# Performance work log

Measured on AMD Instinct MI355X. Metric: run time of the kernel, lower is better.

Reference implementation:

```python
import jax, jax.numpy as jnp
import numpy as np

IN_DIM = 64
HIDDEN = 128
NUM_LAYERS = 2
N_NODES = 10000
N_EDGES = 160000
N_GRAPHS = 32


def _lin_params(key, fan_in, fan_out):
    kw, kb = jax.random.split(key)
    s = 1.0 / np.sqrt(fan_in)
    W = jax.random.uniform(kw, (fan_in, fan_out), jnp.float32, -s, s)
    b = jax.random.uniform(kb, (fan_out,), jnp.float32, -s, s)
    return W, b


def setup_inputs() -> dict:
    key = jax.random.key(0)
    ks = jax.random.split(key, 24)
    H = HIDDEN
    inp = {}
    inp["x1"] = jax.random.normal(ks[0], (N_NODES, IN_DIM), jnp.float32)
    inp["edge_index1"] = jax.random.randint(ks[1], (2, N_EDGES), 0, N_NODES)
    inp["batch1"] = jnp.sort(jax.random.randint(ks[2], (N_NODES,), 0, N_GRAPHS))
    inp["x2"] = jax.random.normal(ks[3], (N_NODES, IN_DIM), jnp.float32)
    inp["edge_index2"] = jax.random.randint(ks[4], (2, N_EDGES), 0, N_NODES)
    inp["batch2"] = jnp.sort(jax.random.randint(ks[5], (N_NODES,), 0, N_GRAPHS))
    # embedding: Linear(in_dim -> hidden)
    inp["W_emb"], inp["b_emb"] = _lin_params(ks[6], IN_DIM, H)
    # per-layer GEMBConv params, stacked over layers
    mW1, mb1, mW2, mb2, uW1, ub1, uW2, ub2 = [], [], [], [], [], [], [], []
    for l in range(NUM_LAYERS):
        k = jax.random.split(ks[7 + l], 4)
        W, b = _lin_params(k[0], 2 * H, 2 * H); mW1.append(W); mb1.append(b)
        W, b = _lin_params(k[1], 2 * H, 2 * H); mW2.append(W); mb2.append(b)
        W, b = _lin_params(k[2], 3 * H, 2 * H); uW1.append(W); ub1.append(b)
        W, b = _lin_params(k[3], 2 * H, H); uW2.append(W); ub2.append(b)
    inp["msg_W1"] = jnp.stack(mW1); inp["msg_b1"] = jnp.stack(mb1)
    inp["msg_W2"] = jnp.stack(mW2); inp["msg_b2"] = jnp.stack(mb2)
    inp["upd_W1"] = jnp.stack(uW1); inp["upd_b1"] = jnp.stack(ub1)
    inp["upd_W2"] = jnp.stack(uW2); inp["upd_b2"] = jnp.stack(ub2)
    # readout: node_net Linear(H -> 2H) (use_gate doubles), graph_net Linear(H -> H)
    inp["node_W"], inp["node_b"] = _lin_params(ks[20], H, 2 * H)
    inp["graph_W"], inp["graph_b"] = _lin_params(ks[21], H, H)
    return inp


def _genet_branch(x, edge_index, batch, W_emb, b_emb,
                  msg_W1, msg_b1, msg_W2, msg_b2,
                  upd_W1, upd_b1, upd_W2, upd_b2,
                  node_W, node_b, graph_W, graph_b):
    H = HIDDEN
    h = x @ W_emb + b_emb  # [N, H]
    tgt, src = edge_index[0], edge_index[1]
    for l in range(NUM_LAYERS):
        # gather-concat: (x[src], x[tgt]) -> [E, 2H]
        mi = jnp.concatenate([h[src], h[tgt]], axis=-1)
        m = jax.nn.relu(mi @ msg_W1[l] + msg_b1[l]) @ msg_W2[l] + msg_b2[l]
        agg = jax.ops.segment_sum(m, tgt, num_segments=N_NODES)  # [N, 2H]
        ui = jnp.concatenate([agg, h], axis=-1)  # [N, 3H]
        u = jax.nn.relu(ui @ upd_W1[l] + upd_b1[l]) @ upd_W2[l] + upd_b2[l]
        h = h + u  # residual node update
    nx = h @ node_W + node_b  # [N, 2H]
    gates = jax.nn.sigmoid(nx[:, :H])
    v = nx[:, H:] * gates
    g = jax.ops.segment_sum(v, batch, num_segments=N_GRAPHS)  # sum pool
    return g @ graph_W + graph_b  # [G, H]


def reference(x1, edge_index1, batch1, x2, edge_index2, batch2,
              W_emb, b_emb, msg_W1, msg_b1, msg_W2, msg_b2,
              upd_W1, upd_b1, upd_W2, upd_b2,
              node_W, node_b, graph_W, graph_b):
    args = (W_emb, b_emb, msg_W1, msg_b1, msg_W2, msg_b2,
            upd_W1, upd_b1, upd_W2, upd_b2, node_W, node_b, graph_W, graph_b)
    embed1 = _genet_branch(x1, edge_index1, batch1, *args)
    embed2 = _genet_branch(x2, edge_index2, batch2, *args)
    return (embed1, embed2)
```

## Files before the change

### kernel.cpp

```cpp
#include <hip/hip_runtime.h>

typedef unsigned short u16;
typedef __bf16 bf16x8 __attribute__((ext_vector_type(8)));
typedef float f32x4 __attribute__((ext_vector_type(4)));
typedef unsigned short u16x8 __attribute__((ext_vector_type(8)));

constexpr int NN  = 10000;
constexpr int NE  = 160000;
constexpr int NG  = 32;
constexpr int HD  = 128;

constexpr size_t WT_PQ   = 0;
constexpr size_t WT_M2R  = 262144;
constexpr size_t WT_UPD1 = 524288;
constexpr size_t WT_U1C  = 917504;
constexpr size_t WT_UPD2 = 1310720;
constexpr size_t WT_NODE = 1441792;
constexpr size_t OFF_C2  = 1507328;
constexpr size_t OFF_DEG = 1509376;
constexpr size_t OFF_ST  = 1589376;
constexpr size_t OFF_CUR = 1669440;
constexpr size_t OFF_SRC = 1749440;
constexpr size_t OFF_H   = 3029440;
constexpr size_t OFF_HB  = 13269440;
constexpr size_t OFF_PQ  = 18389440;
constexpr size_t OFF_UI  = 38869440;
constexpr size_t OFF_G   = 54229440;

__device__ inline u16 f2b(float f) {
  unsigned int u = __float_as_uint(f);
  unsigned int r = u + 0x7fffu + ((u >> 16) & 1u);
  return (u16)(r >> 16);
}
__device__ inline float b2f(u16 u) { return __uint_as_float(((unsigned int)u) << 16); }

__global__ __launch_bounds__(256) void k_prep(
    const float* msgW1, const float* msgW2, const float* updW1,
    const float* updW2, const float* nodeW, const float* msgb2,
    u16* tpq, u16* t2r, u16* t3, u16* tu1c, u16* t4, u16* t5,
    float* c2, int* deg, float* g) {
  int idx = blockIdx.x * 256 + threadIdx.x;
  if (idx < 131072) {
    int l = idx >> 16, r = idx & 65535, n = r >> 7, k = r & 127;
    int row = (n < 256) ? k : (128 + k);
    tpq[idx] = f2b(msgW1[l * 65536 + row * 256 + (n & 255)]);
    t2r[idx] = f2b(msgW2[idx]);
  }
  if (idx < 196608) {
    int l = idx / 98304, r = idx % 98304, n = r / 384, k = r % 384;
    t3[idx] = f2b(updW1[l * 98304 + k * 256 + n]);
  }
  if (idx < 65536) {
    int l = idx >> 15, r = idx & 32767, n = r >> 7, k = r & 127;
    tu1c[l * 98304 + n * 384 + 256 + k] = f2b(updW1[l * 98304 + (256 + k) * 256 + n]);
    int n2 = (idx & 32767) >> 8, k2 = idx & 255;
    t4[idx] = f2b(updW2[(idx >> 15) * 32768 + (k2 << 7) + n2]);
  }
  if (idx < 32768) {
    int n = idx >> 7, k = idx & 127;
    t5[idx] = f2b(nodeW[(k << 8) + n]);
  }
  if (idx < 512) {
    int l = idx >> 8, n = idx & 255;
    const float* b2 = msgb2 + l * 256;
    const float* U1 = updW1 + l * 98304 + n;
    float a = 0.f;
    for (int c = 0; c < 256; c++) a += b2[c] * U1[c * 256];
    c2[idx] = a;
  }
  if (idx < 2 * NN) deg[idx] = 0;
  if (idx < 2 * NG * 128) g[idx] = 0.f;
}

__global__ __launch_bounds__(256) void k_deg(const int* ei0, const int* ei1, int* deg) {
  int br = blockIdx.z;
  int e = blockIdx.x * 256 + threadIdx.x;
  if (e >= NE) return;
  const int* tgt = br ? ei1 : ei0;
  atomicAdd(deg + br * NN + tgt[e], 1);
}

__global__ __launch_bounds__(256) void k_scan(const int* deg, int* starts, int* cursor) {
  int br = blockIdx.z;
  const int* d = deg + br * NN;
  int* st = starts + br * (NN + 8);
  int* cu = cursor + br * NN;
  __shared__ int part[257];
  int t = threadIdx.x;
  int c0 = t * 40;
  int s = 0;
  for (int i = 0; i < 40; i++) if (c0 + i < NN) s += d[c0 + i];
  part[t] = s;
  __syncthreads();
  if (t == 0) {
    int run = 0;
    for (int i = 0; i < 256; i++) { int v = part[i]; part[i] = run; run += v; }
    part[256] = run;
  }
  __syncthreads();
  int run = part[t];
  for (int i = 0; i < 40; i++) {
    int n = c0 + i;
    if (n < NN) { st[n] = run; cu[n] = run; run += d[n]; }
  }
  if (t == 255) st[NN] = part[256];
}

__global__ __launch_bounds__(256) void k_scatter(const int* ei0, const int* ei1,
                                                 int* cursor, int* srcs) {
  int br = blockIdx.z;
  int e = blockIdx.x * 256 + threadIdx.x;
  if (e >= NE) return;
  const int* ei = br ? ei1 : ei0;
  int t = ei[e], s = ei[NE + e];
  int pos = atomicAdd(cursor + br * NN + t, 1);
  srcs[br * NE + pos] = s;
}

__global__ __launch_bounds__(256) void k_embed(
    const float* x1, const float* x2, const float* W, const float* b,
    float* h, u16* h_bf, u16* ui) {
  int br = blockIdx.z;
  const float* x = br ? x2 : x1;
  float* hB = h + (size_t)br * NN * HD;
  u16* hbB = h_bf + (size_t)br * NN * HD;
  u16* uiB = ui + (size_t)br * NN * 384;
  __shared__ float sW[64 * 128];
  __shared__ float sx[32 * 64];
  int tid = threadIdx.x;
  for (int i = tid; i < 64 * 128; i += 256) sW[i] = W[i];
  int r0 = blockIdx.x * 32;
  for (int i = tid; i < 32 * 64; i += 256) {
    int r = i >> 6, k = i & 63;
    sx[i] = (r0 + r < NN) ? x[(size_t)(r0 + r) * 64 + k] : 0.f;
  }
  __syncthreads();
  int c = tid & 127;
  int rbase = (tid >> 7) * 16;
  for (int r = rbase; r < rbase + 16; r++) {
    float acc = b[c];
#pragma unroll
    for (int k = 0; k < 64; k++) acc += sx[r * 64 + k] * sW[k * 128 + c];
    int gr = r0 + r;
    if (gr < NN) {
      u16 bv = f2b(acc);
      hB[(size_t)gr * HD + c] = acc;
      hbB[(size_t)gr * HD + c] = bv;
      uiB[(size_t)gr * 384 + 256 + c] = bv;
    }
  }
}

__global__ __launch_bounds__(256) void k_edge(const u16* PQ, const int* starts,
                                              const int* srcs, const float* b1, u16* ui) {
  int br = blockIdx.z;
  int node = blockIdx.x * 4 + (threadIdx.x >> 6);
  int lane = threadIdx.x & 63;
  int half = lane >> 5;
  int c0 = (lane & 31) * 8;
  const u16* PQb = PQ + (size_t)br * NN * 512;
  const int* st = starts + br * (NN + 8);
  const int* sr = srcs + br * NE;
  u16x8 qr = *(const u16x8*)(PQb + (size_t)node * 512 + 256 + c0);
  float qv[8], acc[8];
#pragma unroll
  for (int j = 0; j < 8; j++) { qv[j] = b2f(qr[j]) + b1[c0 + j]; acc[j] = 0.f; }
  int e0 = st[node], e1 = st[node + 1];
  int e = e0 + half;
  for (; e + 2 < e1; e += 4) {
    int s0 = sr[e], s1 = sr[e + 2];
    u16x8 p0 = *(const u16x8*)(PQb + (size_t)s0 * 512 + c0);
    u16x8 p1 = *(const u16x8*)(PQb + (size_t)s1 * 512 + c0);
#pragma unroll
    for (int j = 0; j < 8; j++) {
      float v0 = b2f(p0[j]) + qv[j];
      float v1 = b2f(p1[j]) + qv[j];
      acc[j] += (v0 > 0.f ? v0 : 0.f) + (v1 > 0.f ? v1 : 0.f);
    }
  }
  for (; e < e1; e += 2) {
    int s0 = sr[e];
    u16x8 p0 = *(const u16x8*)(PQb + (size_t)s0 * 512 + c0);
#pragma unroll
    for (int j = 0; j < 8; j++) {
      float v0 = b2f(p0[j]) + qv[j];
      acc[j] += (v0 > 0.f ? v0 : 0.f);
    }
  }
#pragma unroll
  for (int j = 0; j < 8; j++) acc[j] += __shfl_xor(acc[j], 32);
  if (half == 0) {
    u16x8 o;
#pragma unroll
    for (int j = 0; j < 8; j++) o[j] = f2b(acc[j]);
    *(u16x8*)(ui + (size_t)br * NN * 384 + (size_t)node * 384 + c0) = o;
  }
}

struct GemmP {
  const u16* A;   size_t sA;
  int lda;
  const u16* Wt;  size_t sW;
  u16* outb;  size_t s_outb;
  int M, N, K, ldo;
};

#define LSTR 40

__global__ __launch_bounds__(256) void k_gemm(GemmP p) {
  const int br = blockIdx.z;
  const int tid = threadIdx.x;
  const int lane = tid & 63, wave = tid >> 6;
  const int wm = (wave & 1) * 64, wn = (wave >> 1) * 64;
  const int q = lane >> 4, lr = lane & 15;
  const int m0 = blockIdx.x * 128, n0 = blockIdx.y * 128;
  __shared__ alignas(16) u16 lA[128 * LSTR];
  __shared__ alignas(16) u16 lB[128 * LSTR];

  f32x4 acc[4][4];
#pragma unroll
  for (int i = 0; i < 4; i++)
#pragma unroll
    for (int j = 0; j < 4; j++) acc[i][j] = (f32x4){0.f, 0.f, 0.f, 0.f};

  const u16* Abr = p.A + (size_t)br * p.sA;
  const u16* Wbr = p.Wt + (size_t)br * p.sW;

  for (int k0 = 0; k0 < p.K; k0 += 32) {
#pragma unroll
    for (int c = tid; c < 512; c += 256) {
      int r = c >> 2, kc = (c & 3) << 3;
      int gr = m0 + r;
      u16x8 v = {0, 0, 0, 0, 0, 0, 0, 0};
      if (gr < p.M) v = *(const u16x8*)(Abr + (size_t)gr * p.lda + k0 + kc);
      *(u16x8*)&lA[r * LSTR + kc] = v;
    }
#pragma unroll
    for (int c = tid; c < 512; c += 256) {
      int r = c >> 2, kc = (c & 3) << 3;
      *(u16x8*)&lB[r * LSTR + kc] = *(const u16x8*)(Wbr + (size_t)(n0 + r) * p.K + k0 + kc);
    }
    __syncthreads();
    bf16x8 af[4], bfr[4];
#pragma unroll
    for (int i = 0; i < 4; i++) af[i] = *(const bf16x8*)&lA[(wm + i * 16 + lr) * LSTR + q * 8];
#pragma unroll
    for (int i = 0; i < 4; i++) bfr[i] = *(const bf16x8*)&lB[(wn + i * 16 + lr) * LSTR + q * 8];
#pragma unroll
    for (int mi = 0; mi < 4; mi++)
#pragma unroll
      for (int ni = 0; ni < 4; ni++)
        acc[mi][ni] = __builtin_amdgcn_mfma_f32_16x16x32_bf16(af[mi], bfr[ni], acc[mi][ni], 0, 0, 0);
    __syncthreads();
  }

  u16* ob = p.outb + (size_t)br * p.s_outb;
#pragma unroll
  for (int mi = 0; mi < 4; mi++)
#pragma unroll
    for (int rg = 0; rg < 4; rg++) {
      int row = m0 + wm + mi * 16 + q * 4 + rg;
      if (row >= p.M) continue;
#pragma unroll
      for (int ni = 0; ni < 4; ni++) {
        int col = n0 + wn + ni * 16 + lr;
        ob[(size_t)row * p.ldo + col] = f2b(acc[mi][ni][rg]);
      }
    }
}

__global__ __launch_bounds__(256, 4) void k_upd(
    const u16* ui_all, const u16* w1c, const float* b1u, const float* c2l,
    const int* deg_all, const u16* w2, const float* b2u,
    float* h_all, u16* hb_all) {
  const int br = blockIdx.z;
  const int tid = threadIdx.x;
  const int lane = tid & 63, wave = tid >> 6;
  const int q = lane >> 4, lr = lane & 15;
  const int m0 = blockIdx.x * 32;

  __shared__ alignas(16) u16 sm[32 * LSTR + 256 * LSTR];
  u16* lA = sm;
  u16* lB = sm + 32 * LSTR;
  u16* lU = sm;

  const u16* ui = ui_all + (size_t)br * NN * 384;

  const int wn = wave * 64;
  f32x4 acc[2][4];
#pragma unroll
  for (int i = 0; i < 2; i++)
#pragma unroll
    for (int j = 0; j < 4; j++) acc[i][j] = (f32x4){0.f, 0.f, 0.f, 0.f};

  for (int k0 = 0; k0 < 384; k0 += 32) {
    for (int c = tid; c < 1152; c += 256) {
      if (c < 128) {
        int r = c >> 2, kc = (c & 3) << 3;
        int gr = m0 + r;
        u16x8 v = {0, 0, 0, 0, 0, 0, 0, 0};
        if (gr < NN) v = *(const u16x8*)(ui + (size_t)gr * 384 + k0 + kc);
        *(u16x8*)&lA[r * LSTR + kc] = v;
      } else {
        int cc = c - 128;
        int r = cc >> 2, kc = (cc & 3) << 3;
        *(u16x8*)&lB[r * LSTR + kc] = *(const u16x8*)(w1c + (size_t)r * 384 + k0 + kc);
      }
    }
    __syncthreads();
    bf16x8 af[2], bfr[4];
#pragma unroll
    for (int i = 0; i < 2; i++) af[i] = *(const bf16x8*)&lA[(i * 16 + lr) * LSTR + q * 8];
#pragma unroll
    for (int i = 0; i < 4; i++) bfr[i] = *(const bf16x8*)&lB[(wn + i * 16 + lr) * LSTR + q * 8];
#pragma unroll
    for (int mi = 0; mi < 2; mi++)
#pragma unroll
      for (int ni = 0; ni < 4; ni++)
        acc[mi][ni] = __builtin_amdgcn_mfma_f32_16x16x32_bf16(af[mi], bfr[ni], acc[mi][ni], 0, 0, 0);
    __syncthreads();
  }

  const int* deg = deg_all + br * NN;
#pragma unroll
  for (int mi = 0; mi < 2; mi++)
#pragma unroll
    for (int rg = 0; rg < 4; rg++) {
      int row = mi * 16 + q * 4 + rg;
      int gr = m0 + row;
      float d = (gr < NN) ? (float)deg[gr] : 0.f;
#pragma unroll
      for (int ni = 0; ni < 4; ni++) {
        int col = wn + ni * 16 + lr;
        float v = acc[mi][ni][rg] + b1u[col] + d * c2l[col];
        if (v < 0.f) v = 0.f;
        lU[row * 272 + col] = f2b(v);
      }
    }
  __syncthreads();

  const int wn2 = wave * 32;
  f32x4 acc2[2][2];
#pragma unroll
  for (int i = 0; i < 2; i++)
#pragma unroll
    for (int j = 0; j < 2; j++) acc2[i][j] = (f32x4){0.f, 0.f, 0.f, 0.f};

  for (int k0 = 0; k0 < 256; k0 += 32) {
    bf16x8 af[2], bfr[2];
#pragma unroll
    for (int i = 0; i < 2; i++)
      af[i] = *(const bf16x8*)&lU[(i * 16 + lr) * 272 + k0 + q * 8];
#pragma unroll
    for (int i = 0; i < 2; i++)
      bfr[i] = *(const bf16x8*)(w2 + (size_t)(wn2 + i * 16 + lr) * 256 + k0 + q * 8);
#pragma unroll
    for (int mi = 0; mi < 2; mi++)
#pragma unroll
      for (int ni = 0; ni < 2; ni++)
        acc2[mi][ni] = __builtin_amdgcn_mfma_f32_16x16x32_bf16(af[mi], bfr[ni], acc2[mi][ni], 0, 0, 0);
  }

  float* h = h_all + (size_t)br * NN * 128;
  u16* hb = hb_all + (size_t)br * NN * 128;
  u16* uiw = (u16*)ui_all + (size_t)br * NN * 384;
#pragma unroll
  for (int mi = 0; mi < 2; mi++)
#pragma unroll
    for (int rg = 0; rg < 4; rg++) {
      int row = m0 + mi * 16 + q * 4 + rg;
      if (row >= NN) continue;
#pragma unroll
      for (int ni = 0; ni < 2; ni++) {
        int col = wn2 + ni * 16 + lr;
        size_t o = (size_t)row * 128 + col;
        float nh = h[o] + acc2[mi][ni][rg] + b2u[col];
        u16 bv = f2b(nh);
        h[o] = nh;
        hb[o] = bv;
        uiw[(size_t)row * 384 + 256 + col] = bv;
      }
    }
}

__global__ __launch_bounds__(256, 4) void k_nxg(
    const u16* hb_all, const u16* wnode, const float* nb,
    const int* b0v, const int* b1v, float* g) {
  const int br = blockIdx.z;
  const int tid = threadIdx.x;
  const int lane = tid & 63, wave = tid >> 6;
  const int q = lane >> 4, lr = lane & 15;
  const int m0 = blockIdx.x * 64;
  const int wg = wave * 32;

  __shared__ alignas(16) u16 lA[64 * LSTR];
  __shared__ alignas(16) u16 lB[256 * LSTR];
  __shared__ int sbat[64];

  const u16* hb = hb_all + (size_t)br * NN * 128;
  const int* batch = br ? b1v : b0v;
  if (tid < 64) {
    int n = m0 + tid;
    sbat[tid] = (n < NN) ? batch[n] : -1;
  }

  f32x4 acc[4][4];
#pragma unroll
  for (int i = 0; i < 4; i++)
#pragma unroll
    for (int j = 0; j < 4; j++) acc[i][j] = (f32x4){0.f, 0.f, 0.f, 0.f};

  for (int k0 = 0; k0 < 128; k0 += 32) {
    for (int c = tid; c < 1280; c += 256) {
      if (c < 256) {
        int r = c >> 2, kc = (c & 3) << 3;
        int gr = m0 + r;
        u16x8 v = {0, 0, 0, 0, 0, 0, 0, 0};
        if (gr < NN) v = *(const u16x8*)(hb + (size_t)gr * 128 + k0 + kc);
        *(u16x8*)&lA[r * LSTR + kc] = v;
      } else {
        int cc = c - 256;
        int r = cc >> 2, kc = (cc & 3) << 3;
        *(u16x8*)&lB[r * LSTR + kc] = *(const u16x8*)(wnode + (size_t)r * 128 + k0 + kc);
      }
    }
    __syncthreads();
    bf16x8 af[4], bfr[4];
#pragma unroll
    for (int i = 0; i < 4; i++) af[i] = *(const bf16x8*)&lA[(i * 16 + lr) * LSTR + q * 8];
#pragma unroll
    for (int i = 0; i < 4; i++) {
      int nrow = (i < 2) ? (wg + i * 16 + lr) : (128 + wg + (i - 2) * 16 + lr);
      bfr[i] = *(const bf16x8*)&lB[nrow * LSTR + q * 8];
    }
#pragma unroll
    for (int mi = 0; mi < 4; mi++)
#pragma unroll
      for (int ni = 0; ni < 4; ni++)
        acc[mi][ni] = __builtin_amdgcn_mfma_f32_16x16x32_bf16(af[mi], bfr[ni], acc[mi][ni], 0, 0, 0);
    __syncthreads();
  }

  float* gb = g + (size_t)br * NG * 128;
  float racc[2] = {0.f, 0.f};
  int cur = -1;
#pragma unroll
  for (int mi = 0; mi < 4; mi++)
#pragma unroll
    for (int rg = 0; rg < 4; rg++) {
      int lrow = mi * 16 + q * 4 + rg;
      int bt = sbat[lrow];
      if (bt != cur) {
        if (cur >= 0) {
#pragma unroll
          for (int ni = 0; ni < 2; ni++)
            atomicAdd(gb + (size_t)cur * 128 + wg + ni * 16 + lr, racc[ni]);
        }
        cur = bt;
        racc[0] = 0.f; racc[1] = 0.f;
      }
      if (bt >= 0) {
#pragma unroll
        for (int ni = 0; ni < 2; ni++) {
          int gcol = wg + ni * 16 + lr;
          float gt = acc[mi][ni][rg] + nb[gcol];
          float vl = acc[mi][ni + 2][rg] + nb[128 + gcol];
          racc[ni] += vl / (1.f + __expf(-gt));
        }
      }
    }
  if (cur >= 0) {
#pragma unroll
    for (int ni = 0; ni < 2; ni++)
      atomicAdd(gb + (size_t)cur * 128 + wg + ni * 16 + lr, racc[ni]);
  }
}

__global__ __launch_bounds__(128) void k_final(const float* g, const float* W,
                                               const float* b, float* out) {
  int br = blockIdx.z, gi = blockIdx.x, j = threadIdx.x;
  __shared__ float sg[128];
  sg[j] = g[(size_t)br * NG * 128 + (size_t)gi * 128 + j];
  __syncthreads();
  float acc = b[j];
#pragma unroll
  for (int k = 0; k < 128; k++) acc += sg[k] * W[k * 128 + j];
  out[(size_t)br * NG * 128 + (size_t)gi * 128 + j] = acc;
}

extern "C" void kernel_launch(void* const* d_in, const int* in_sizes, int n_in,
                              void* d_out, int out_size, void* d_ws, size_t ws_size,
                              hipStream_t stream) {
  const float* x1     = (const float*)d_in[0];
  const int*   ei1    = (const int*)d_in[1];
  const int*   bat1   = (const int*)d_in[2];
  const float* x2     = (const float*)d_in[3];
  const int*   ei2    = (const int*)d_in[4];
  const int*   bat2   = (const int*)d_in[5];
  const float* W_emb  = (const float*)d_in[6];
  const float* b_emb  = (const float*)d_in[7];
  const float* msg_W1 = (const float*)d_in[8];
  const float* msg_b1 = (const float*)d_in[9];
  const float* msg_W2 = (const float*)d_in[10];
  const float* msg_b2 = (const float*)d_in[11];
  const float* upd_W1 = (const float*)d_in[12];
  const float* upd_b1 = (const float*)d_in[13];
  const float* upd_W2 = (const float*)d_in[14];
  const float* upd_b2 = (const float*)d_in[15];
  const float* node_W = (const float*)d_in[16];
  const float* node_b = (const float*)d_in[17];
  const float* graph_W = (const float*)d_in[18];
  const float* graph_b = (const float*)d_in[19];
  float* out = (float*)d_out;

  char* ws = (char*)d_ws;
  u16* wt_pq   = (u16*)(ws + WT_PQ);
  u16* wt_m2r  = (u16*)(ws + WT_M2R);
  u16* wt_upd1 = (u16*)(ws + WT_UPD1);
  u16* wt_u1c  = (u16*)(ws + WT_U1C);
  u16* wt_upd2 = (u16*)(ws + WT_UPD2);
  u16* wt_node = (u16*)(ws + WT_NODE);
  float* c2    = (float*)(ws + OFF_C2);
  int* deg    = (int*)(ws + OFF_DEG);
  int* starts = (int*)(ws + OFF_ST);
  int* cursor = (int*)(ws + OFF_CUR);
  int* srcs   = (int*)(ws + OFF_SRC);
  float* h  = (float*)(ws + OFF_H);
  u16*   hb = (u16*)(ws + OFF_HB);
  u16*   PQ = (u16*)(ws + OFF_PQ);
  u16*   ui = (u16*)(ws + OFF_UI);
  float* g  = (float*)(ws + OFF_G);

  k_prep<<<768, 256, 0, stream>>>(msg_W1, msg_W2, upd_W1, upd_W2, node_W, msg_b2,
                                  wt_pq, wt_m2r, wt_upd1, wt_u1c, wt_upd2, wt_node,
                                  c2, deg, g);
  {
    GemmP pc{};
    pc.A = wt_upd1; pc.sA = 98304; pc.lda = 384;
    pc.Wt = wt_m2r; pc.sW = 65536;
    pc.outb = wt_u1c; pc.s_outb = 98304;
    pc.M = 256; pc.N = 256; pc.K = 256; pc.ldo = 384;
    k_gemm<<<dim3(2, 2, 2), 256, 0, stream>>>(pc);
  }
  k_deg<<<dim3(625, 1, 2), 256, 0, stream>>>(ei1, ei2, deg);
  k_scan<<<dim3(1, 1, 2), 256, 0, stream>>>(deg, starts, cursor);
  k_scatter<<<dim3(625, 1, 2), 256, 0, stream>>>(ei1, ei2, cursor, srcs);
  k_embed<<<dim3(313, 1, 2), 256, 0, stream>>>(x1, x2, W_emb, b_emb, h, hb, ui);

  for (int l = 0; l < 2; l++) {
    GemmP pq{};
    pq.A = hb; pq.sA = (size_t)NN * 128; pq.lda = 128;
    pq.Wt = wt_pq + (size_t)l * 65536; pq.sW = 0;
    pq.outb = PQ; pq.s_outb = (size_t)NN * 512;
    pq.M = NN; pq.N = 512; pq.K = 128; pq.ldo = 512;
    k_gemm<<<dim3(79, 4, 2), 256, 0, stream>>>(pq);

    k_edge<<<dim3(2500, 1, 2), 256, 0, stream>>>(PQ, starts, srcs, msg_b1 + l * 256, ui);

    k_upd<<<dim3(313, 1, 2), 256, 0, stream>>>(
        ui, wt_u1c + (size_t)l * 98304, upd_b1 + l * 256, c2 + l * 256,
        deg, wt_upd2 + (size_t)l * 32768, upd_b2 + l * 128, h, hb);
  }

  k_nxg<<<dim3(157, 1, 2), 256, 0, stream>>>(hb, wt_node, node_b, bat1, bat2, g);
  k_final<<<dim3(NG, 1, 2), 128, 0, stream>>>(g, graph_W, graph_b, out);
}
```

Measured before the change: 372.1 us.

## Fuse PQ projection into embed/update kernels and node readout into last update

Removes the standalone PQ GEMM launches by computing the per-node PQ projection inside k_embed and k_upd from the freshly computed bf16 h tile held in shared memory. The readout (node_net GEMM, gating and segment pooling) is fused into the final layer's k_upd through a mode flag, and k_nxg is dropped. The intent is to save launches and the re-read of hb from global memory. k_edge also changes from interleaved halves to contiguous halves with a 4-wide unroll. In exchange, k_upd uses more shared memory and runs with lower occupancy (launch bound 3), and the fused GEMMs load weights directly from global memory without LDS staging.

```diff
diff --git a/kernel.cpp b/kernel.cpp
--- a/kernel.cpp
+++ b/kernel.cpp
@@ -27,6 +27,8 @@
 constexpr size_t OFF_UI  = 38869440;
 constexpr size_t OFF_G   = 54229440;
 
+#define LSTR 40
+
 __device__ inline u16 f2b(float f) {
   unsigned int u = __float_as_uint(f);
   unsigned int r = u + 0x7fffu + ((u >> 16) & 1u);
@@ -117,9 +119,46 @@
   srcs[br * NE + pos] = s;
 }
 
+__device__ __forceinline__ void pq_from_lhb(
+    const u16* lhb, const u16* wq, u16* PQ, int m0, int wave, int lane) {
+  const int q = lane >> 4, lr = lane & 15;
+  f32x4 a3[2][8];
+#pragma unroll
+  for (int i = 0; i < 2; i++)
+#pragma unroll
+    for (int j = 0; j < 8; j++) a3[i][j] = (f32x4){0.f, 0.f, 0.f, 0.f};
+#pragma unroll
+  for (int k0 = 0; k0 < 128; k0 += 32) {
+    bf16x8 af[2], bfr[8];
+#pragma unroll
+    for (int i = 0; i < 2; i++)
+      af[i] = *(const bf16x8*)&lhb[(i * 16 + lr) * 136 + k0 + q * 8];
+#pragma unroll
+    for (int i = 0; i < 8; i++)
+      bfr[i] = *(const bf16x8*)(wq + (size_t)(wave * 128 + i * 16 + lr) * 128 + k0 + q * 8);
+#pragma unroll
+    for (int mi = 0; mi < 2; mi++)
+#pragma unroll
+      for (int ni = 0; ni < 8; ni++)
+        a3[mi][ni] = __builtin_amdgcn_mfma_f32_16x16x32_bf16(af[mi], bfr[ni], a3[mi][ni], 0, 0, 0);
+  }
+#pragma unroll
+  for (int mi = 0; mi < 2; mi++)
+#pragma unroll
+    for (int rg = 0; rg < 4; rg++) {
+      int grow = m0 + mi * 16 + q * 4 + rg;
+      if (grow >= NN) continue;
+#pragma unroll
+      for (int ni = 0; ni < 8; ni++) {
+        int col = wave * 128 + ni * 16 + lr;
+        PQ[(size_t)grow * 512 + col] = f2b(a3[mi][ni][rg]);
+      }
+    }
+}
+
 __global__ __launch_bounds__(256) void k_embed(
     const float* x1, const float* x2, const float* W, const float* b,
-    float* h, u16* h_bf, u16* ui) {
+    float* h, u16* h_bf, u16* ui, const u16* wpq0, u16* PQ_all) {
   int br = blockIdx.z;
   const float* x = br ? x2 : x1;
   float* hB = h + (size_t)br * NN * HD;
@@ -127,6 +166,7 @@
   u16* uiB = ui + (size_t)br * NN * 384;
   __shared__ float sW[64 * 128];
   __shared__ float sx[32 * 64];
+  __shared__ alignas(16) u16 lhb[32 * 136];
   int tid = threadIdx.x;
   for (int i = tid; i < 64 * 128; i += 256) sW[i] = W[i];
   int r0 = blockIdx.x * 32;
@@ -142,13 +182,16 @@
 #pragma unroll
     for (int k = 0; k < 64; k++) acc += sx[r * 64 + k] * sW[k * 128 + c];
     int gr = r0 + r;
+    u16 bv = f2b(acc);
+    lhb[r * 136 + c] = bv;
     if (gr < NN) {
-      u16 bv = f2b(acc);
       hB[(size_t)gr * HD + c] = acc;
       hbB[(size_t)gr * HD + c] = bv;
       uiB[(size_t)gr * 384 + 256 + c] = bv;
     }
   }
+  __syncthreads();
+  pq_from_lhb(lhb, wpq0, PQ_all + (size_t)br * NN * 512, r0, tid >> 6, tid & 63);
 }
 
 __global__ __launch_bounds__(256) void k_edge(const u16* PQ, const int* starts,
@@ -166,9 +209,27 @@
 #pragma unroll
   for (int j = 0; j < 8; j++) { qv[j] = b2f(qr[j]) + b1[c0 + j]; acc[j] = 0.f; }
   int e0 = st[node], e1 = st[node + 1];
-  int e = e0 + half;
-  for (; e + 2 < e1; e += 4) {
-    int s0 = sr[e], s1 = sr[e + 2];
+  int mid = e0 + ((e1 - e0 + 1) >> 1);
+  int e = half ? mid : e0;
+  int ee = half ? e1 : mid;
+  for (; e + 3 < ee; e += 4) {
+    int s0 = sr[e], s1 = sr[e + 1], s2 = sr[e + 2], s3 = sr[e + 3];
+    u16x8 p0 = *(const u16x8*)(PQb + (size_t)s0 * 512 + c0);
+    u16x8 p1 = *(const u16x8*)(PQb + (size_t)s1 * 512 + c0);
+    u16x8 p2 = *(const u16x8*)(PQb + (size_t)s2 * 512 + c0);
+    u16x8 p3 = *(const u16x8*)(PQb + (size_t)s3 * 512 + c0);
+#pragma unroll
+    for (int j = 0; j < 8; j++) {
+      float v0 = b2f(p0[j]) + qv[j];
+      float v1 = b2f(p1[j]) + qv[j];
+      float v2 = b2f(p2[j]) + qv[j];
+      float v3 = b2f(p3[j]) + qv[j];
+      acc[j] += (v0 > 0.f ? v0 : 0.f) + (v1 > 0.f ? v1 : 0.f)
+              + (v2 > 0.f ? v2 : 0.f) + (v3 > 0.f ? v3 : 0.f);
+    }
+  }
+  for (; e + 1 < ee; e += 2) {
+    int s0 = sr[e], s1 = sr[e + 1];
     u16x8 p0 = *(const u16x8*)(PQb + (size_t)s0 * 512 + c0);
     u16x8 p1 = *(const u16x8*)(PQb + (size_t)s1 * 512 + c0);
 #pragma unroll
@@ -178,7 +239,7 @@
       acc[j] += (v0 > 0.f ? v0 : 0.f) + (v1 > 0.f ? v1 : 0.f);
     }
   }
-  for (; e < e1; e += 2) {
+  if (e < ee) {
     int s0 = sr[e];
     u16x8 p0 = *(const u16x8*)(PQb + (size_t)s0 * 512 + c0);
 #pragma unroll
@@ -204,8 +265,6 @@
   u16* outb;  size_t s_outb;
   int M, N, K, ldo;
 };
-
-#define LSTR 40
 
 __global__ __launch_bounds__(256) void k_gemm(GemmP p) {
   const int br = blockIdx.z;
@@ -269,20 +328,30 @@
     }
 }
 
-__global__ __launch_bounds__(256, 4) void k_upd(
+__global__ __launch_bounds__(256, 3) void k_upd(
     const u16* ui_all, const u16* w1c, const float* b1u, const float* c2l,
     const int* deg_all, const u16* w2, const float* b2u,
-    float* h_all, u16* hb_all) {
+    float* h_all, u16* hb_all, int mode,
+    const u16* wpq_next, u16* PQ_all,
+    const u16* wnode, const float* nb, const int* b0v, const int* b1v, float* g) {
   const int br = blockIdx.z;
   const int tid = threadIdx.x;
   const int lane = tid & 63, wave = tid >> 6;
   const int q = lane >> 4, lr = lane & 15;
   const int m0 = blockIdx.x * 32;
 
-  __shared__ alignas(16) u16 sm[32 * LSTR + 256 * LSTR];
+  __shared__ alignas(16) u16 sm[32 * LSTR + 256 * LSTR + 32 * 136];
+  __shared__ int sbat[32];
   u16* lA = sm;
   u16* lB = sm + 32 * LSTR;
   u16* lU = sm;
+  u16* lhb = sm + 32 * LSTR + 256 * LSTR;
+
+  if (mode == 1 && tid < 32) {
+    const int* batch = br ? b1v : b0v;
+    int n = m0 + tid;
+    sbat[tid] = (n < NN) ? batch[n] : -1;
+  }
 
   const u16* ui = ui_all + (size_t)br * NN * 384;
 
@@ -368,111 +437,85 @@
   for (int mi = 0; mi < 2; mi++)
 #pragma unroll
     for (int rg = 0; rg < 4; rg++) {
-      int row = m0 + mi * 16 + q * 4 + rg;
-      if (row >= NN) continue;
+      int lrow = mi * 16 + q * 4 + rg;
+      int grow = m0 + lrow;
 #pragma unroll
       for (int ni = 0; ni < 2; ni++) {
         int col = wn2 + ni * 16 + lr;
-        size_t o = (size_t)row * 128 + col;
-        float nh = h[o] + acc2[mi][ni][rg] + b2u[col];
-        u16 bv = f2b(nh);
-        h[o] = nh;
-        hb[o] = bv;
-        uiw[(size_t)row * 384 + 256 + col] = bv;
-      }
-    }
-}
-
-__global__ __launch_bounds__(256, 4) void k_nxg(
-    const u16* hb_all, const u16* wnode, const float* nb,
-    const int* b0v, const int* b1v, float* g) {
-  const int br = blockIdx.z;
-  const int tid = threadIdx.x;
-  const int lane = tid & 63, wave = tid >> 6;
-  const int q = lane >> 4, lr = lane & 15;
-  const int m0 = blockIdx.x * 64;
-  const int wg = wave * 32;
-
-  __shared__ alignas(16) u16 lA[64 * LSTR];
-  __shared__ alignas(16) u16 lB[256 * LSTR];
-  __shared__ int sbat[64];
-
-  const u16* hb = hb_all + (size_t)br * NN * 128;
-  const int* batch = br ? b1v : b0v;
-  if (tid < 64) {
-    int n = m0 + tid;
-    sbat[tid] = (n < NN) ? batch[n] : -1;
-  }
-
-  f32x4 acc[4][4];
-#pragma unroll
-  for (int i = 0; i < 4; i++)
-#pragma unroll
-    for (int j = 0; j < 4; j++) acc[i][j] = (f32x4){0.f, 0.f, 0.f, 0.f};
-
-  for (int k0 = 0; k0 < 128; k0 += 32) {
-    for (int c = tid; c < 1280; c += 256) {
-      if (c < 256) {
-        int r = c >> 2, kc = (c & 3) << 3;
-        int gr = m0 + r;
-        u16x8 v = {0, 0, 0, 0, 0, 0, 0, 0};
-        if (gr < NN) v = *(const u16x8*)(hb + (size_t)gr * 128 + k0 + kc);
-        *(u16x8*)&lA[r * LSTR + kc] = v;
-      } else {
-        int cc = c - 256;
-        int r = cc >> 2, kc = (cc & 3) << 3;
-        *(u16x8*)&lB[r * LSTR + kc] = *(const u16x8*)(wnode + (size_t)r * 128 + k0 + kc);
-      }
-    }
-    __syncthreads();
-    bf16x8 af[4], bfr[4];
-#pragma unroll
-    for (int i = 0; i < 4; i++) af[i] = *(const bf16x8*)&lA[(i * 16 + lr) * LSTR + q * 8];
-#pragma unroll
-    for (int i = 0; i < 4; i++) {
-      int nrow = (i < 2) ? (wg + i * 16 + lr) : (128 + wg + (i - 2) * 16 + lr);
-      bfr[i] = *(const bf16x8*)&lB[nrow * LSTR + q * 8];
-    }
-#pragma unroll
-    for (int mi = 0; mi < 4; mi++)
-#pragma unroll
-      for (int ni = 0; ni < 4; ni++)
-        acc[mi][ni] = __builtin_amdgcn_mfma_f32_16x16x32_bf16(af[mi], bfr[ni], acc[mi][ni], 0, 0, 0);
-    __syncthreads();
-  }
-
-  float* gb = g + (size_t)br * NG * 128;
-  float racc[2] = {0.f, 0.f};
-  int cur = -1;
-#pragma unroll
-  for (int mi = 0; mi < 4; mi++)
-#pragma unroll
-    for (int rg = 0; rg < 4; rg++) {
-      int lrow = mi * 16 + q * 4 + rg;
-      int bt = sbat[lrow];
-      if (bt != cur) {
-        if (cur >= 0) {
-#pragma unroll
-          for (int ni = 0; ni < 2; ni++)
-            atomicAdd(gb + (size_t)cur * 128 + wg + ni * 16 + lr, racc[ni]);
-        }
-        cur = bt;
-        racc[0] = 0.f; racc[1] = 0.f;
-      }
-      if (bt >= 0) {
-#pragma unroll
-        for (int ni = 0; ni < 2; ni++) {
-          int gcol = wg + ni * 16 + lr;
-          float gt = acc[mi][ni][rg] + nb[gcol];
-          float vl = acc[mi][ni + 2][rg] + nb[128 + gcol];
-          racc[ni] += vl / (1.f + __expf(-gt));
+        if (grow < NN) {
+          size_t o = (size_t)grow * 128 + col;
+          float nh = h[o] + acc2[mi][ni][rg] + b2u[col];
+          u16 bv = f2b(nh);
+          h[o] = nh;
+          hb[o] = bv;
+          uiw[(size_t)grow * 384 + 256 + col] = bv;
+          lhb[lrow * 136 + col] = bv;
+        } else {
+          lhb[lrow * 136 + col] = 0;
         }
       }
     }
-  if (cur >= 0) {
-#pragma unroll
-    for (int ni = 0; ni < 2; ni++)
-      atomicAdd(gb + (size_t)cur * 128 + wg + ni * 16 + lr, racc[ni]);
+  __syncthreads();
+
+  if (mode == 0) {
+    pq_from_lhb(lhb, wpq_next, PQ_all + (size_t)br * NN * 512, m0, wave, lane);
+  } else {
+    const int wg = wave * 32;
+    f32x4 a3[2][4];
+#pragma unroll
+    for (int i = 0; i < 2; i++)
+#pragma unroll
+      for (int j = 0; j < 4; j++) a3[i][j] = (f32x4){0.f, 0.f, 0.f, 0.f};
+#pragma unroll
+    for (int k0 = 0; k0 < 128; k0 += 32) {
+      bf16x8 af[2], bfr[4];
+#pragma unroll
+      for (int i = 0; i < 2; i++)
+        af[i] = *(const bf16x8*)&lhb[(i * 16 + lr) * 136 + k0 + q * 8];
+#pragma unroll
+      for (int i = 0; i < 4; i++) {
+        int nrow = (i < 2) ? (wg + i * 16 + lr) : (128 + wg + (i - 2) * 16 + lr);
+        bfr[i] = *(const bf16x8*)(wnode + (size_t)nrow * 128 + k0 + q * 8);
+      }
+#pragma unroll
+      for (int mi = 0; mi < 2; mi++)
+#pragma unroll
+        for (int ni = 0; ni < 4; ni++)
+          a3[mi][ni] = __builtin_amdgcn_mfma_f32_16x16x32_bf16(af[mi], bfr[ni], a3[mi][ni], 0, 0, 0);
+    }
+    float* gb = g + (size_t)br * NG * 128;
+    float racc[2] = {0.f, 0.f};
+    int cur = -1;
+#pragma unroll
+    for (int mi = 0; mi < 2; mi++)
+#pragma unroll
+      for (int rg = 0; rg < 4; rg++) {
+        int lrow = mi * 16 + q * 4 + rg;
+        int bt = sbat[lrow];
+        if (bt != cur) {
+          if (cur >= 0) {
+#pragma unroll
+            for (int ni = 0; ni < 2; ni++)
+              atomicAdd(gb + (size_t)cur * 128 + wg + ni * 16 + lr, racc[ni]);
+          }
+          cur = bt;
+          racc[0] = 0.f; racc[1] = 0.f;
+        }
+        if (bt >= 0) {
+#pragma unroll
+          for (int ni = 0; ni < 2; ni++) {
+            int gcol = wg + ni * 16 + lr;
+            float gt = a3[mi][ni][rg] + nb[gcol];
+            float vl = a3[mi][ni + 2][rg] + nb[128 + gcol];
+            racc[ni] += vl / (1.f + __expf(-gt));
+          }
+        }
+      }
+    if (cur >= 0) {
+#pragma unroll
+      for (int ni = 0; ni < 2; ni++)
+        atomicAdd(gb + (size_t)cur * 128 + wg + ni * 16 + lr, racc[ni]);
+    }
   }
 }
 
@@ -545,23 +588,19 @@
   k_deg<<<dim3(625, 1, 2), 256, 0, stream>>>(ei1, ei2, deg);
   k_scan<<<dim3(1, 1, 2), 256, 0, stream>>>(deg, starts, cursor);
   k_scatter<<<dim3(625, 1, 2), 256, 0, stream>>>(ei1, ei2, cursor, srcs);
-  k_embed<<<dim3(313, 1, 2), 256, 0, stream>>>(x1, x2, W_emb, b_emb, h, hb, ui);
+  k_embed<<<dim3(313, 1, 2), 256, 0, stream>>>(x1, x2, W_emb, b_emb, h, hb, ui,
+                                               wt_pq, PQ);
 
   for (int l = 0; l < 2; l++) {
-    GemmP pq{};
-    pq.A = hb; pq.sA = (size_t)NN * 128; pq.lda = 128;
-    pq.Wt = wt_pq + (size_t)l * 65536; pq.sW = 0;
-    pq.outb = PQ; pq.s_outb = (size_t)NN * 512;
-    pq.M = NN; pq.N = 512; pq.K = 128; pq.ldo = 512;
-    k_gemm<<<dim3(79, 4, 2), 256, 0, stream>>>(pq);
-
     k_edge<<<dim3(2500, 1, 2), 256, 0, stream>>>(PQ, starts, srcs, msg_b1 + l * 256, ui);
 
     k_upd<<<dim3(313, 1, 2), 256, 0, stream>>>(
         ui, wt_u1c + (size_t)l * 98304, upd_b1 + l * 256, c2 + l * 256,
-        deg, wt_upd2 + (size_t)l * 32768, upd_b2 + l * 128, h, hb);
-  }
-
-  k_nxg<<<dim3(157, 1, 2), 256, 0, stream>>>(hb, wt_node, node_b, bat1, bat2, g);
+        deg, wt_upd2 + (size_t)l * 32768, upd_b2 + l * 128, h, hb,
+        (l == 0) ? 0 : 1,
+        wt_pq + 65536, PQ,
+        wt_node, node_b, bat1, bat2, g);
+  }
+
   k_final<<<dim3(NG, 1, 2), 128, 0, stream>>>(g, graph_W, graph_b, out);
 }
```

Result: faster. 362.8 us (-2.5%).
